# Performance work log

Hardware: AMD Instinct MI355X
Metric: run time of the kernel (lower is better)

Reference implementation:

```python
import jax, jax.numpy as jnp
import numpy as np

DIM = 768
HEADS = 12
DIM_HEAD = 64
INNER = HEADS * DIM_HEAD  # 768
EPS = 1e-5


def setup_inputs() -> dict:
    key = jax.random.key(0)
    ks = jax.random.split(key, 5)
    x = jax.random.normal(ks[0], (4, 2048, DIM), dtype=jnp.float32)
    ln_g = jnp.ones((DIM,), dtype=jnp.float32)
    ln_b = jnp.zeros((DIM,), dtype=jnp.float32)
    s1 = 1.0 / np.sqrt(DIM)
    W_qkv = jax.random.uniform(ks[1], (DIM, 3 * INNER), dtype=jnp.float32, minval=-s1, maxval=s1)
    b_qkv = jax.random.uniform(ks[2], (3 * INNER,), dtype=jnp.float32, minval=-s1, maxval=s1)
    s2 = 1.0 / np.sqrt(INNER)
    W_out = jax.random.uniform(ks[3], (INNER, DIM), dtype=jnp.float32, minval=-s2, maxval=s2)
    b_out = jax.random.uniform(ks[4], (DIM,), dtype=jnp.float32, minval=-s2, maxval=s2)
    return {"x": x, "ln_g": ln_g, "ln_b": ln_b, "W_qkv": W_qkv, "b_qkv": b_qkv, "W_out": W_out, "b_out": b_out}


def reference(x, ln_g, ln_b, W_qkv, b_qkv, W_out, b_out):
    b, n, _ = x.shape
    # pre-norm LayerNorm
    mu = jnp.mean(x, axis=-1, keepdims=True)
    var = jnp.mean(jnp.square(x - mu), axis=-1, keepdims=True)
    xn = (x - mu) * jax.lax.rsqrt(var + EPS) * ln_g + ln_b
    qkv = xn @ W_qkv + b_qkv  # [b, n, 3*inner]
    q, k, v = jnp.split(qkv, 3, axis=-1)
    def to_heads(t):
        return t.reshape(b, n, HEADS, DIM_HEAD).transpose(0, 2, 1, 3)  # b h n d
    q, k, v = map(to_heads, (q, k, v))
    q = q * (DIM_HEAD ** -0.5)
    sim = jnp.einsum('bhid,bhjd->bhij', q, k)
    attn = jax.nn.softmax(sim, axis=-1)  # dropout is identity (p=0.0)
    out = jnp.einsum('bhij,bhjd->bhid', attn, v)
    out = out.transpose(0, 2, 1, 3).reshape(b, n, INNER)
    return out @ W_out + b_out
```

## Files before the change

kernel.cpp:

```cpp
#include <hip/hip_runtime.h>
#include <cstdint>
#include <cstddef>


#define SEQ    2048
#define NBATCH 4
#define DMODEL 768
#define NHEADS 12
#define DHEAD  64
#define MROWS  (NBATCH * SEQ)
#define NQKV   (3 * DMODEL)
#define KT     64
#define NT     (SEQ / KT)

using f32x4  = __attribute__((ext_vector_type(4))) float;
using u16x8  = __attribute__((ext_vector_type(8))) unsigned short;
using s16x8  = __attribute__((ext_vector_type(8))) short;
using u16x4  = __attribute__((ext_vector_type(4))) unsigned short;
using s16x4  = __attribute__((ext_vector_type(4))) short;

__device__ __forceinline__ unsigned short f2bf(float f) {
  union { float f; unsigned int u; } x; x.f = f;
  unsigned int r = x.u + 0x7fffu + ((x.u >> 16) & 1u);
  return (unsigned short)(r >> 16);
}

#if defined(__has_builtin)
#if __has_builtin(__builtin_amdgcn_cvt_pk_bf16_f32)
#define HAVE_PK_BF16 1
#endif
#if __has_builtin(__builtin_amdgcn_exp2f)
#define HAVE_EXP2 1
#endif
#if __has_builtin(__builtin_amdgcn_mfma_f32_16x16x16bf16_1k)
#define HAVE_MFMA_16X16X16_BF16 1
#endif
#endif

__device__ __forceinline__ unsigned int pk_bf16(float a, float b) {
#ifdef HAVE_PK_BF16
  auto v = __builtin_amdgcn_cvt_pk_bf16_f32(a, b);
  union { decltype(v) v2; unsigned int u; } c; c.v2 = v; return c.u;
#else
  return (unsigned int)f2bf(a) | ((unsigned int)f2bf(b) << 16);
#endif
}

__device__ __forceinline__ float fexp2(float x) {
#ifdef HAVE_EXP2
  return __builtin_amdgcn_exp2f(x);
#else
  return exp2f(x);
#endif
}

__device__ __forceinline__ f32x4 mfma16(u16x8 a, u16x8 b, f32x4 c) {
  return __builtin_amdgcn_mfma_f32_16x16x32_bf16((s16x8)a, (s16x8)b, c, 0, 0, 0);
}

__device__ __forceinline__ f32x4 mfma16k16(u16x4 a, u16x4 b, f32x4 c) {
#ifdef HAVE_MFMA_16X16X16_BF16
  return __builtin_amdgcn_mfma_f32_16x16x16bf16_1k((s16x4)a, (s16x4)b, c, 0, 0, 0);
#else
  f32x4 d;
  asm("v_mfma_f32_16x16x16_bf16 %0, %1, %2, %3"
      : "=v"(d) : "v"(a), "v"(b), "v"(c));
  return d;
#endif
}

__device__ __forceinline__ void gl_lds16(const void* g, void* l) {
  __builtin_amdgcn_global_load_lds(
      (const __attribute__((address_space(1))) void*)g,
      (__attribute__((address_space(3))) void*)l, 16, 0, 0);
}

__global__ __launch_bounds__(256) void ln_kernel(
    const float* __restrict__ x, const float* __restrict__ g,
    const float* __restrict__ bb, unsigned short* __restrict__ xn) {
  __shared__ float red[8];
  const int row = blockIdx.x, t = threadIdx.x;
  const float* xr = x + (size_t)row * DMODEL;
  float v0 = xr[t], v1 = xr[t + 256], v2 = xr[t + 512];
  float s = v0 + v1 + v2;
#pragma unroll
  for (int o = 32; o; o >>= 1) s += __shfl_down(s, o);
  if ((t & 63) == 0) red[t >> 6] = s;
  __syncthreads();
  float mu = (red[0] + red[1] + red[2] + red[3]) * (1.0f / DMODEL);
  float d0 = v0 - mu, d1 = v1 - mu, d2 = v2 - mu;
  float q = d0 * d0 + d1 * d1 + d2 * d2;
#pragma unroll
  for (int o = 32; o; o >>= 1) q += __shfl_down(q, o);
  if ((t & 63) == 0) red[4 + (t >> 6)] = q;
  __syncthreads();
  float var = (red[4] + red[5] + red[6] + red[7]) * (1.0f / DMODEL);
  float rstd = rsqrtf(var + 1e-5f);
  size_t base = (size_t)row * DMODEL;
  xn[base + t]       = f2bf(d0 * rstd * g[t]       + bb[t]);
  xn[base + t + 256] = f2bf(d1 * rstd * g[t + 256] + bb[t + 256]);
  xn[base + t + 512] = f2bf(d2 * rstd * g[t + 512] + bb[t + 512]);
}

__global__ __launch_bounds__(256) void tconv_kernel(
    const float* __restrict__ W, unsigned short* __restrict__ Wt, int N) {
  __shared__ float tile[32][33];
  const int n0 = blockIdx.x * 32, k0 = blockIdx.y * 32;
  const int tx = threadIdx.x & 31, ty = threadIdx.x >> 5;
#pragma unroll
  for (int r = 0; r < 4; ++r)
    tile[ty + r * 8][tx] = W[(size_t)(k0 + ty + r * 8) * N + n0 + tx];
  __syncthreads();
#pragma unroll
  for (int r = 0; r < 4; ++r)
    Wt[(size_t)(n0 + ty + r * 8) * DMODEL + k0 + tx] = f2bf(tile[tx][ty + r * 8]);
}

__global__ __launch_bounds__(256, 2) void gemm_qk_kernel(
    const unsigned short* __restrict__ Wt, const unsigned short* __restrict__ xn,
    const float* __restrict__ bias, unsigned short* __restrict__ qb,
    unsigned short* __restrict__ kb) {
  __shared__ alignas(16) unsigned short As[128 * 64];
  __shared__ alignas(16) unsigned short Bs[128 * 64];
  const int t = threadIdx.x, wid = t >> 6, l = t & 63, quad = l >> 4, ll = l & 15;
  const int a0 = blockIdx.x * 128;
  const int b0 = blockIdx.y * 128;
  const int wa = (wid >> 1) * 64, wb = (wid & 1) * 64;
  const int srow = l >> 3, sblk = (l & 7) ^ srow;
  f32x4 acc[4][4] = {};
  for (int k0 = 0; k0 < DMODEL; k0 += 64) {
#pragma unroll
    for (int cc = 0; cc < 4; ++cc) {
      int call = wid * 4 + cc;
      int r = call * 8 + srow;
      gl_lds16(Wt + (size_t)(a0 + r) * DMODEL + k0 + sblk * 8, &As[call * 512]);
      gl_lds16(xn + (size_t)(b0 + r) * DMODEL + k0 + sblk * 8, &Bs[call * 512]);
    }
    __syncthreads();
#pragma unroll
    for (int ks = 0; ks < 2; ++ks) {
      u16x8 af[4], bf[4];
#pragma unroll
      for (int i = 0; i < 4; ++i) {
        int ra = wa + i * 16 + ll, rb = wb + i * 16 + ll;
        int blk = (ks * 4 + quad) ^ (ll & 7);
        af[i] = *(const u16x8*)&As[ra * 64 + blk * 8];
        bf[i] = *(const u16x8*)&Bs[rb * 64 + blk * 8];
      }
#pragma unroll
      for (int mi = 0; mi < 4; ++mi)
#pragma unroll
        for (int ni = 0; ni < 4; ++ni)
          acc[mi][ni] = mfma16(af[mi], bf[ni], acc[mi][ni]);
    }
    __syncthreads();
  }
  const bool isq = (a0 < DMODEL);
  unsigned short* dst = isq ? qb : kb;
  const float sc = isq ? 0.18033688f : 1.0f;
#pragma unroll
  for (int mi = 0; mi < 4; ++mi) {
    int row0 = a0 + wa + mi * 16 + quad * 4;
    float4 bv = *(const float4*)&bias[row0];
    int rr = isq ? row0 : row0 - DMODEL;
    int h = rr >> 6, d0 = rr & 63;
#pragma unroll
    for (int ni = 0; ni < 4; ++ni) {
      int seq = b0 + wb + ni * 16 + ll;
      int b = seq >> 11, i = seq & 2047;
      uint2 pk;
      pk.x = pk_bf16((acc[mi][ni][0] + bv.x) * sc, (acc[mi][ni][1] + bv.y) * sc);
      pk.y = pk_bf16((acc[mi][ni][2] + bv.z) * sc, (acc[mi][ni][3] + bv.w) * sc);
      *(uint2*)&dst[(size_t)((b * NHEADS + h) * SEQ + i) * DHEAD + d0] = pk;
    }
  }
}

__global__ __launch_bounds__(256, 2) void gemm_v_kernel(
    const unsigned short* __restrict__ A, const unsigned short* __restrict__ Bt,
    const float* __restrict__ bias, unsigned short* __restrict__ vt) {
  __shared__ alignas(16) unsigned short As[128 * 64];
  __shared__ alignas(16) unsigned short Bs[128 * 64];
  const int t = threadIdx.x, wid = t >> 6, l = t & 63, quad = l >> 4, ll = l & 15;
  const int m0 = blockIdx.x * 128;
  const int n0 = 2 * DMODEL + blockIdx.y * 128;
  const int wm = (wid >> 1) * 64, wn = (wid & 1) * 64;
  const int srow = l >> 3, sblk = (l & 7) ^ srow;
  f32x4 acc[4][4] = {};
  for (int k0 = 0; k0 < DMODEL; k0 += 64) {
#pragma unroll
    for (int cc = 0; cc < 4; ++cc) {
      int call = wid * 4 + cc;
      int r = call * 8 + srow;
      gl_lds16(A  + (size_t)(m0 + r) * DMODEL + k0 + sblk * 8, &As[call * 512]);
      gl_lds16(Bt + (size_t)(n0 + r) * DMODEL + k0 + sblk * 8, &Bs[call * 512]);
    }
    __syncthreads();
#pragma unroll
    for (int ks = 0; ks < 2; ++ks) {
      u16x8 af[4], bf[4];
#pragma unroll
      for (int i = 0; i < 4; ++i) {
        int ra = wm + i * 16 + ll, rb = wn + i * 16 + ll;
        int blk = (ks * 4 + quad) ^ (ll & 7);
        af[i] = *(const u16x8*)&As[ra * 64 + blk * 8];
        bf[i] = *(const u16x8*)&Bs[rb * 64 + blk * 8];
      }
#pragma unroll
      for (int mi = 0; mi < 4; ++mi)
#pragma unroll
        for (int ni = 0; ni < 4; ++ni)
          acc[mi][ni] = mfma16(af[mi], bf[ni], acc[mi][ni]);
    }
    __syncthreads();
  }
#pragma unroll
  for (int mi = 0; mi < 4; ++mi) {
    int gm = m0 + wm + mi * 16 + quad * 4;
    int b = gm >> 11, i0 = gm & 2047;
#pragma unroll
    for (int ni = 0; ni < 4; ++ni) {
      int gn = n0 + wn + ni * 16 + ll;
      float bv = bias[gn];
      int rem = gn - 2 * DMODEL;
      int h = rem >> 6, d = rem & 63;
      int bh = b * NHEADS + h;
      uint2 pk;
      pk.x = pk_bf16(acc[mi][ni][0] + bv, acc[mi][ni][1] + bv);
      pk.y = pk_bf16(acc[mi][ni][2] + bv, acc[mi][ni][3] + bv);
      *(uint2*)&vt[((size_t)bh * DHEAD + d) * SEQ + i0] = pk;
    }
  }
}

__global__ __launch_bounds__(256, 3) void attn_kernel(
    const unsigned short* __restrict__ qbuf, const unsigned short* __restrict__ kbuf,
    const unsigned short* __restrict__ vtg, unsigned short* __restrict__ ao) {
  __shared__ alignas(16) unsigned short stage[2][2][KT * DHEAD];
  const int t = threadIdx.x, wid = t >> 6, l = t & 63, quad = l >> 4, ll = l & 15;
  const int Lid = blockIdx.y * 16 + blockIdx.x;
  const int w = (Lid & 7) * 96 + (Lid >> 3);
  const int qt = w & 15, bh = w >> 4;
  const unsigned short* qg  = qbuf + ((size_t)bh * SEQ + qt * 128) * DHEAD;
  const unsigned short* kg0 = kbuf + (size_t)bh * SEQ * DHEAD;
  const unsigned short* vt0 = vtg  + (size_t)bh * DHEAD * SEQ;
  const int srow = l >> 3;
  const int sblk = (l & 7) ^ srow;

  unsigned short* Qs = &stage[0][0][0];
#pragma unroll
  for (int cc = 0; cc < 4; ++cc) {
    int call = wid * 4 + cc;
    gl_lds16(qg + (call * 8 + srow) * 64 + sblk * 8, Qs + call * 512);
  }
  __syncthreads();
  u16x8 qf[2][2];
#pragma unroll
  for (int mi = 0; mi < 2; ++mi)
#pragma unroll
    for (int ks = 0; ks < 2; ++ks) {
      int r = wid * 32 + mi * 16 + ll;
      int blk = (ks * 4 + quad) ^ (ll & 7);
      qf[mi][ks] = *(const u16x8*)&Qs[r * 64 + blk * 8];
    }
  __syncthreads();

  auto stage_tile = [&](int buf, int kt2) {
    const unsigned short* kg = kg0 + (size_t)kt2 * KT * DHEAD;
#pragma unroll
    for (int c = 0; c < 2; ++c) {
      int call = wid * 2 + c;
      int r = call * 8 + srow;
      gl_lds16(kg + r * 64 + sblk * 8, &stage[buf][0][call * 512]);
      gl_lds16(vt0 + (size_t)r * SEQ + kt2 * KT + sblk * 8, &stage[buf][1][call * 512]);
    }
  };

  f32x4 oacc[2][4] = {};
  f32x4 osum[2] = {};
  const u16x4 onesb = {0x3f80u, 0x3f80u, 0x3f80u, 0x3f80u};

  stage_tile(0, 0);
  int buf = 0;
  for (int kt2 = 0; kt2 < NT; ++kt2) {
    __syncthreads();
    if (kt2 + 1 < NT) stage_tile(buf ^ 1, kt2 + 1);
    const unsigned short* Ks = &stage[buf][0][0];
    const unsigned short* Vs = &stage[buf][1][0];

    f32x4 st[2][4] = {};
#pragma unroll
    for (int ks = 0; ks < 2; ++ks)
#pragma unroll
      for (int ni = 0; ni < 4; ++ni) {
        int r = ni * 16 + ll;
        int blk = (ks * 4 + quad) ^ (ll & 7);
        u16x8 kf = *(const u16x8*)&Ks[r * 64 + blk * 8];
        st[0][ni] = mfma16(kf, qf[0][ks], st[0][ni]);
        st[1][ni] = mfma16(kf, qf[1][ks], st[1][ni]);
      }

#pragma unroll
    for (int ni = 0; ni < 4; ++ni) {
      u16x4 pf[2];
#pragma unroll
      for (int mi = 0; mi < 2; ++mi) {
        float p0 = fexp2(st[mi][ni][0]);
        float p1 = fexp2(st[mi][ni][1]);
        float p2 = fexp2(st[mi][ni][2]);
        float p3 = fexp2(st[mi][ni][3]);
        union { uint2 u; u16x4 v; } cv;
        cv.u.x = pk_bf16(p0, p1);
        cv.u.y = pk_bf16(p2, p3);
        pf[mi] = cv.v;
        osum[mi] = mfma16k16(pf[mi], onesb, osum[mi]);
      }
      const int voff = (((ni * 2 + (quad >> 1)) ^ (ll & 7)) << 3) + (quad & 1) * 4;
#pragma unroll
      for (int di = 0; di < 4; ++di) {
        u16x4 vf = *(const u16x4*)&Vs[(di * 16 + ll) * 64 + voff];
        oacc[0][di] = mfma16k16(pf[0], vf, oacc[0][di]);
        oacc[1][di] = mfma16k16(pf[1], vf, oacc[1][di]);
      }
    }
    buf ^= 1;
  }

  const int b = bh / NHEADS, h = bh - b * NHEADS;
#pragma unroll
  for (int mi = 0; mi < 2; ++mi) {
#pragma unroll
    for (int r = 0; r < 4; ++r) {
      float inv = 1.0f / osum[mi][r];
      int row = qt * 128 + wid * 32 + mi * 16 + quad * 4 + r;
      size_t base = ((size_t)(b * SEQ + row)) * DMODEL + h * DHEAD;
#pragma unroll
      for (int di = 0; di < 4; ++di)
        ao[base + di * 16 + ll] = f2bf(oacc[mi][di][r] * inv);
    }
  }
}

__global__ __launch_bounds__(256, 2) void gemm_out_kernel(
    const unsigned short* __restrict__ Wt, const unsigned short* __restrict__ ao,
    const float* __restrict__ bias, float* __restrict__ out) {
  __shared__ alignas(16) unsigned short As[128 * 64];
  __shared__ alignas(16) unsigned short Bs[128 * 64];
  const int t = threadIdx.x, wid = t >> 6, l = t & 63, quad = l >> 4, ll = l & 15;
  const int a0 = blockIdx.x * 128;
  const int b0 = blockIdx.y * 128;
  const int wa = (wid >> 1) * 64, wb = (wid & 1) * 64;
  const int srow = l >> 3, sblk = (l & 7) ^ srow;
  f32x4 acc[4][4] = {};
  for (int k0 = 0; k0 < DMODEL; k0 += 64) {
#pragma unroll
    for (int cc = 0; cc < 4; ++cc) {
      int call = wid * 4 + cc;
      int r = call * 8 + srow;
      gl_lds16(Wt + (size_t)(a0 + r) * DMODEL + k0 + sblk * 8, &As[call * 512]);
      gl_lds16(ao + (size_t)(b0 + r) * DMODEL + k0 + sblk * 8, &Bs[call * 512]);
    }
    __syncthreads();
#pragma unroll
    for (int ks = 0; ks < 2; ++ks) {
      u16x8 af[4], bf[4];
#pragma unroll
      for (int i = 0; i < 4; ++i) {
        int ra = wa + i * 16 + ll, rb = wb + i * 16 + ll;
        int blk = (ks * 4 + quad) ^ (ll & 7);
        af[i] = *(const u16x8*)&As[ra * 64 + blk * 8];
        bf[i] = *(const u16x8*)&Bs[rb * 64 + blk * 8];
      }
#pragma unroll
      for (int mi = 0; mi < 4; ++mi)
#pragma unroll
        for (int ni = 0; ni < 4; ++ni)
          acc[mi][ni] = mfma16(af[mi], bf[ni], acc[mi][ni]);
    }
    __syncthreads();
  }
#pragma unroll
  for (int mi = 0; mi < 4; ++mi) {
    int row0 = a0 + wa + mi * 16 + quad * 4;
    float4 bv = *(const float4*)&bias[row0];
#pragma unroll
    for (int ni = 0; ni < 4; ++ni) {
      int seq = b0 + wb + ni * 16 + ll;
      float4 o;
      o.x = acc[mi][ni][0] + bv.x;
      o.y = acc[mi][ni][1] + bv.y;
      o.z = acc[mi][ni][2] + bv.z;
      o.w = acc[mi][ni][3] + bv.w;
      *(float4*)&out[(size_t)seq * DMODEL + row0] = o;
    }
  }
}

extern "C" void kernel_launch(void* const* d_in, const int* in_sizes, int n_in,
                              void* d_out, int out_size, void* d_ws, size_t ws_size,
                              hipStream_t stream) {
  const float* x     = (const float*)d_in[0];
  const float* ln_g  = (const float*)d_in[1];
  const float* ln_b  = (const float*)d_in[2];
  const float* W_qkv = (const float*)d_in[3];
  const float* b_qkv = (const float*)d_in[4];
  const float* W_out = (const float*)d_in[5];
  const float* b_out = (const float*)d_in[6];
  float* out = (float*)d_out;

  char* ws = (char*)d_ws;
  unsigned short* xn    = (unsigned short*)(ws);
  unsigned short* wqkvt = (unsigned short*)(ws + 12582912);
  unsigned short* woutt = (unsigned short*)(ws + 16121856);
  unsigned short* qb    = (unsigned short*)(ws + 17301504);
  unsigned short* kb    = (unsigned short*)(ws + 29884416);
  unsigned short* vt    = (unsigned short*)(ws + 42467328);
  unsigned short* ao    = xn;

  ln_kernel<<<MROWS, 256, 0, stream>>>(x, ln_g, ln_b, xn);
  tconv_kernel<<<dim3(NQKV / 32, DMODEL / 32), 256, 0, stream>>>(W_qkv, wqkvt, NQKV);
  tconv_kernel<<<dim3(DMODEL / 32, DMODEL / 32), 256, 0, stream>>>(W_out, woutt, DMODEL);
  gemm_qk_kernel<<<dim3(12, 64), 256, 0, stream>>>(wqkvt, xn, b_qkv, qb, kb);
  gemm_v_kernel<<<dim3(64, 6), 256, 0, stream>>>(xn, wqkvt, b_qkv, vt);
  attn_kernel<<<dim3(SEQ / 128, NBATCH * NHEADS), 256, 0, stream>>>(qb, kb, vt, ao);
  gemm_out_kernel<<<dim3(6, 64), 256, 0, stream>>>(woutt, ao, b_out, out);
}
```

Before: 247.4 us.

## Merge QK and V GEMMs, widen attention blocks to 8 waves, halve out-GEMM tile

Folds the separate QK and V projection GEMMs into one launch of 1152 blocks with a remapped block index, removing a launch and the tail gap between them. The attention kernel now runs 512 threads per block, with each wave owning 16 query rows instead of 32. This cuts per-wave registers and raises occupancy, at the cost of less K/V reuse per wave. The output GEMM uses 64x128 tiles to double the block count and fill more CUs, which gives lower arithmetic intensity per tile.

```diff
diff --git a/kernel.cpp b/kernel.cpp
--- a/kernel.cpp
+++ b/kernel.cpp
@@ -116,15 +116,21 @@
     Wt[(size_t)(n0 + ty + r * 8) * DMODEL + k0 + tx] = f2bf(tile[tx][ty + r * 8]);
 }
 
-__global__ __launch_bounds__(256, 2) void gemm_qk_kernel(
+__global__ __launch_bounds__(256, 2) void gemm_qkv_kernel(
     const unsigned short* __restrict__ Wt, const unsigned short* __restrict__ xn,
     const float* __restrict__ bias, unsigned short* __restrict__ qb,
-    unsigned short* __restrict__ kb) {
+    unsigned short* __restrict__ kb, unsigned short* __restrict__ vt) {
   __shared__ alignas(16) unsigned short As[128 * 64];
   __shared__ alignas(16) unsigned short Bs[128 * 64];
   const int t = threadIdx.x, wid = t >> 6, l = t & 63, quad = l >> 4, ll = l & 15;
-  const int a0 = blockIdx.x * 128;
-  const int b0 = blockIdx.y * 128;
+  const int bid = blockIdx.x;
+  const int w = (bid & 7) * 144 + (bid >> 3);
+  const bool isqk = (w < 768);
+  int a0, b0;
+  if (isqk) { a0 = (w % 12) * 128; b0 = (w / 12) * 128; }
+  else { int w2 = w - 768; a0 = (w2 & 63) * 128; b0 = 2 * DMODEL + (w2 >> 6) * 128; }
+  const unsigned short* Ap = isqk ? (Wt + (size_t)a0 * DMODEL) : (xn + (size_t)a0 * DMODEL);
+  const unsigned short* Bp = isqk ? (xn + (size_t)b0 * DMODEL) : (Wt + (size_t)b0 * DMODEL);
   const int wa = (wid >> 1) * 64, wb = (wid & 1) * 64;
   const int srow = l >> 3, sblk = (l & 7) ^ srow;
   f32x4 acc[4][4] = {};
@@ -133,8 +139,8 @@
     for (int cc = 0; cc < 4; ++cc) {
       int call = wid * 4 + cc;
       int r = call * 8 + srow;
-      gl_lds16(Wt + (size_t)(a0 + r) * DMODEL + k0 + sblk * 8, &As[call * 512]);
-      gl_lds16(xn + (size_t)(b0 + r) * DMODEL + k0 + sblk * 8, &Bs[call * 512]);
+      gl_lds16(Ap + (size_t)r * DMODEL + k0 + sblk * 8, &As[call * 512]);
+      gl_lds16(Bp + (size_t)r * DMODEL + k0 + sblk * 8, &Bs[call * 512]);
     }
     __syncthreads();
 #pragma unroll
@@ -155,85 +161,48 @@
     }
     __syncthreads();
   }
-  const bool isq = (a0 < DMODEL);
-  unsigned short* dst = isq ? qb : kb;
-  const float sc = isq ? 0.18033688f : 1.0f;
-#pragma unroll
-  for (int mi = 0; mi < 4; ++mi) {
-    int row0 = a0 + wa + mi * 16 + quad * 4;
-    float4 bv = *(const float4*)&bias[row0];
-    int rr = isq ? row0 : row0 - DMODEL;
-    int h = rr >> 6, d0 = rr & 63;
-#pragma unroll
-    for (int ni = 0; ni < 4; ++ni) {
-      int seq = b0 + wb + ni * 16 + ll;
-      int b = seq >> 11, i = seq & 2047;
-      uint2 pk;
-      pk.x = pk_bf16((acc[mi][ni][0] + bv.x) * sc, (acc[mi][ni][1] + bv.y) * sc);
-      pk.y = pk_bf16((acc[mi][ni][2] + bv.z) * sc, (acc[mi][ni][3] + bv.w) * sc);
-      *(uint2*)&dst[(size_t)((b * NHEADS + h) * SEQ + i) * DHEAD + d0] = pk;
-    }
-  }
-}
-
-__global__ __launch_bounds__(256, 2) void gemm_v_kernel(
-    const unsigned short* __restrict__ A, const unsigned short* __restrict__ Bt,
-    const float* __restrict__ bias, unsigned short* __restrict__ vt) {
-  __shared__ alignas(16) unsigned short As[128 * 64];
-  __shared__ alignas(16) unsigned short Bs[128 * 64];
-  const int t = threadIdx.x, wid = t >> 6, l = t & 63, quad = l >> 4, ll = l & 15;
-  const int m0 = blockIdx.x * 128;
-  const int n0 = 2 * DMODEL + blockIdx.y * 128;
-  const int wm = (wid >> 1) * 64, wn = (wid & 1) * 64;
-  const int srow = l >> 3, sblk = (l & 7) ^ srow;
-  f32x4 acc[4][4] = {};
-  for (int k0 = 0; k0 < DMODEL; k0 += 64) {
-#pragma unroll
-    for (int cc = 0; cc < 4; ++cc) {
-      int call = wid * 4 + cc;
-      int r = call * 8 + srow;
-      gl_lds16(A  + (size_t)(m0 + r) * DMODEL + k0 + sblk * 8, &As[call * 512]);
-      gl_lds16(Bt + (size_t)(n0 + r) * DMODEL + k0 + sblk * 8, &Bs[call * 512]);
-    }
-    __syncthreads();
-#pragma unroll
-    for (int ks = 0; ks < 2; ++ks) {
-      u16x8 af[4], bf[4];
-#pragma unroll
-      for (int i = 0; i < 4; ++i) {
-        int ra = wm + i * 16 + ll, rb = wn + i * 16 + ll;
-        int blk = (ks * 4 + quad) ^ (ll & 7);
-        af[i] = *(const u16x8*)&As[ra * 64 + blk * 8];
-        bf[i] = *(const u16x8*)&Bs[rb * 64 + blk * 8];
-      }
-#pragma unroll
-      for (int mi = 0; mi < 4; ++mi)
-#pragma unroll
-        for (int ni = 0; ni < 4; ++ni)
-          acc[mi][ni] = mfma16(af[mi], bf[ni], acc[mi][ni]);
-    }
-    __syncthreads();
-  }
-#pragma unroll
-  for (int mi = 0; mi < 4; ++mi) {
-    int gm = m0 + wm + mi * 16 + quad * 4;
-    int b = gm >> 11, i0 = gm & 2047;
-#pragma unroll
-    for (int ni = 0; ni < 4; ++ni) {
-      int gn = n0 + wn + ni * 16 + ll;
-      float bv = bias[gn];
-      int rem = gn - 2 * DMODEL;
-      int h = rem >> 6, d = rem & 63;
-      int bh = b * NHEADS + h;
-      uint2 pk;
-      pk.x = pk_bf16(acc[mi][ni][0] + bv, acc[mi][ni][1] + bv);
-      pk.y = pk_bf16(acc[mi][ni][2] + bv, acc[mi][ni][3] + bv);
-      *(uint2*)&vt[((size_t)bh * DHEAD + d) * SEQ + i0] = pk;
-    }
-  }
-}
-
-__global__ __launch_bounds__(256, 3) void attn_kernel(
+  if (isqk) {
+    const bool isq = (a0 < DMODEL);
+    unsigned short* dst = isq ? qb : kb;
+    const float sc = isq ? 0.18033688f : 1.0f;
+#pragma unroll
+    for (int mi = 0; mi < 4; ++mi) {
+      int row0 = a0 + wa + mi * 16 + quad * 4;
+      float4 bv = *(const float4*)&bias[row0];
+      int rr = isq ? row0 : row0 - DMODEL;
+      int h = rr >> 6, d0 = rr & 63;
+#pragma unroll
+      for (int ni = 0; ni < 4; ++ni) {
+        int seq = b0 + wb + ni * 16 + ll;
+        int b = seq >> 11, i = seq & 2047;
+        uint2 pk;
+        pk.x = pk_bf16((acc[mi][ni][0] + bv.x) * sc, (acc[mi][ni][1] + bv.y) * sc);
+        pk.y = pk_bf16((acc[mi][ni][2] + bv.z) * sc, (acc[mi][ni][3] + bv.w) * sc);
+        *(uint2*)&dst[(size_t)((b * NHEADS + h) * SEQ + i) * DHEAD + d0] = pk;
+      }
+    }
+  } else {
+#pragma unroll
+    for (int mi = 0; mi < 4; ++mi) {
+      int gm = a0 + wa + mi * 16 + quad * 4;
+      int b = gm >> 11, i0 = gm & 2047;
+#pragma unroll
+      for (int ni = 0; ni < 4; ++ni) {
+        int gn = b0 + wb + ni * 16 + ll;
+        float bv = bias[gn];
+        int rem = gn - 2 * DMODEL;
+        int h = rem >> 6, d = rem & 63;
+        int bh = b * NHEADS + h;
+        uint2 pk;
+        pk.x = pk_bf16(acc[mi][ni][0] + bv, acc[mi][ni][1] + bv);
+        pk.y = pk_bf16(acc[mi][ni][2] + bv, acc[mi][ni][3] + bv);
+        *(uint2*)&vt[((size_t)bh * DHEAD + d) * SEQ + i0] = pk;
+      }
+    }
+  }
+}
+
+__global__ __launch_bounds__(512, 6) void attn_kernel(
     const unsigned short* __restrict__ qbuf, const unsigned short* __restrict__ kbuf,
     const unsigned short* __restrict__ vtg, unsigned short* __restrict__ ao) {
   __shared__ alignas(16) unsigned short stage[2][2][KT * DHEAD];
@@ -249,35 +218,29 @@
 
   unsigned short* Qs = &stage[0][0][0];
 #pragma unroll
-  for (int cc = 0; cc < 4; ++cc) {
-    int call = wid * 4 + cc;
+  for (int cc = 0; cc < 2; ++cc) {
+    int call = wid * 2 + cc;
     gl_lds16(qg + (call * 8 + srow) * 64 + sblk * 8, Qs + call * 512);
   }
   __syncthreads();
-  u16x8 qf[2][2];
-#pragma unroll
-  for (int mi = 0; mi < 2; ++mi)
-#pragma unroll
-    for (int ks = 0; ks < 2; ++ks) {
-      int r = wid * 32 + mi * 16 + ll;
-      int blk = (ks * 4 + quad) ^ (ll & 7);
-      qf[mi][ks] = *(const u16x8*)&Qs[r * 64 + blk * 8];
-    }
+  u16x8 qf[2];
+#pragma unroll
+  for (int ks = 0; ks < 2; ++ks) {
+    int r = wid * 16 + ll;
+    int blk = (ks * 4 + quad) ^ (ll & 7);
+    qf[ks] = *(const u16x8*)&Qs[r * 64 + blk * 8];
+  }
   __syncthreads();
 
   auto stage_tile = [&](int buf, int kt2) {
     const unsigned short* kg = kg0 + (size_t)kt2 * KT * DHEAD;
-#pragma unroll
-    for (int c = 0; c < 2; ++c) {
-      int call = wid * 2 + c;
-      int r = call * 8 + srow;
-      gl_lds16(kg + r * 64 + sblk * 8, &stage[buf][0][call * 512]);
-      gl_lds16(vt0 + (size_t)r * SEQ + kt2 * KT + sblk * 8, &stage[buf][1][call * 512]);
-    }
+    int r = wid * 8 + srow;
+    gl_lds16(kg + r * 64 + sblk * 8, &stage[buf][0][wid * 512]);
+    gl_lds16(vt0 + (size_t)r * SEQ + kt2 * KT + sblk * 8, &stage[buf][1][wid * 512]);
   };
 
-  f32x4 oacc[2][4] = {};
-  f32x4 osum[2] = {};
+  f32x4 oacc[4] = {};
+  f32x4 osum = {};
   const u16x4 onesb = {0x3f80u, 0x3f80u, 0x3f80u, 0x3f80u};
 
   stage_tile(0, 0);
@@ -288,7 +251,7 @@
     const unsigned short* Ks = &stage[buf][0][0];
     const unsigned short* Vs = &stage[buf][1][0];
 
-    f32x4 st[2][4] = {};
+    f32x4 st[4] = {};
 #pragma unroll
     for (int ks = 0; ks < 2; ++ks)
 #pragma unroll
@@ -296,31 +259,25 @@
         int r = ni * 16 + ll;
         int blk = (ks * 4 + quad) ^ (ll & 7);
         u16x8 kf = *(const u16x8*)&Ks[r * 64 + blk * 8];
-        st[0][ni] = mfma16(kf, qf[0][ks], st[0][ni]);
-        st[1][ni] = mfma16(kf, qf[1][ks], st[1][ni]);
+        st[ni] = mfma16(kf, qf[ks], st[ni]);
       }
 
 #pragma unroll
     for (int ni = 0; ni < 4; ++ni) {
-      u16x4 pf[2];
-#pragma unroll
-      for (int mi = 0; mi < 2; ++mi) {
-        float p0 = fexp2(st[mi][ni][0]);
-        float p1 = fexp2(st[mi][ni][1]);
-        float p2 = fexp2(st[mi][ni][2]);
-        float p3 = fexp2(st[mi][ni][3]);
-        union { uint2 u; u16x4 v; } cv;
-        cv.u.x = pk_bf16(p0, p1);
-        cv.u.y = pk_bf16(p2, p3);
-        pf[mi] = cv.v;
-        osum[mi] = mfma16k16(pf[mi], onesb, osum[mi]);
-      }
+      float p0 = fexp2(st[ni][0]);
+      float p1 = fexp2(st[ni][1]);
+      float p2 = fexp2(st[ni][2]);
+      float p3 = fexp2(st[ni][3]);
+      union { uint2 u; u16x4 v; } cv;
+      cv.u.x = pk_bf16(p0, p1);
+      cv.u.y = pk_bf16(p2, p3);
+      u16x4 pf = cv.v;
+      osum = mfma16k16(pf, onesb, osum);
       const int voff = (((ni * 2 + (quad >> 1)) ^ (ll & 7)) << 3) + (quad & 1) * 4;
 #pragma unroll
       for (int di = 0; di < 4; ++di) {
         u16x4 vf = *(const u16x4*)&Vs[(di * 16 + ll) * 64 + voff];
-        oacc[0][di] = mfma16k16(pf[0], vf, oacc[0][di]);
-        oacc[1][di] = mfma16k16(pf[1], vf, oacc[1][di]);
+        oacc[di] = mfma16k16(pf, vf, oacc[di]);
       }
     }
     buf ^= 1;
@@ -328,51 +285,58 @@
 
   const int b = bh / NHEADS, h = bh - b * NHEADS;
 #pragma unroll
-  for (int mi = 0; mi < 2; ++mi) {
-#pragma unroll
-    for (int r = 0; r < 4; ++r) {
-      float inv = 1.0f / osum[mi][r];
-      int row = qt * 128 + wid * 32 + mi * 16 + quad * 4 + r;
-      size_t base = ((size_t)(b * SEQ + row)) * DMODEL + h * DHEAD;
-#pragma unroll
-      for (int di = 0; di < 4; ++di)
-        ao[base + di * 16 + ll] = f2bf(oacc[mi][di][r] * inv);
-    }
-  }
-}
-
-__global__ __launch_bounds__(256, 2) void gemm_out_kernel(
+  for (int r = 0; r < 4; ++r) {
+    float inv = 1.0f / osum[r];
+    int row = qt * 128 + wid * 16 + quad * 4 + r;
+    size_t base = ((size_t)(b * SEQ + row)) * DMODEL + h * DHEAD;
+#pragma unroll
+    for (int di = 0; di < 4; ++di)
+      ao[base + di * 16 + ll] = f2bf(oacc[di][r] * inv);
+  }
+}
+
+__global__ __launch_bounds__(256, 3) void gemm_out_kernel(
     const unsigned short* __restrict__ Wt, const unsigned short* __restrict__ ao,
     const float* __restrict__ bias, float* __restrict__ out) {
-  __shared__ alignas(16) unsigned short As[128 * 64];
+  __shared__ alignas(16) unsigned short As[64 * 64];
   __shared__ alignas(16) unsigned short Bs[128 * 64];
   const int t = threadIdx.x, wid = t >> 6, l = t & 63, quad = l >> 4, ll = l & 15;
-  const int a0 = blockIdx.x * 128;
+  const int a0 = blockIdx.x * 64;
   const int b0 = blockIdx.y * 128;
-  const int wa = (wid >> 1) * 64, wb = (wid & 1) * 64;
+  const int wa = (wid >> 1) * 32, wb = (wid & 1) * 64;
   const int srow = l >> 3, sblk = (l & 7) ^ srow;
-  f32x4 acc[4][4] = {};
+  f32x4 acc[2][4] = {};
   for (int k0 = 0; k0 < DMODEL; k0 += 64) {
 #pragma unroll
-    for (int cc = 0; cc < 4; ++cc) {
-      int call = wid * 4 + cc;
-      int r = call * 8 + srow;
-      gl_lds16(Wt + (size_t)(a0 + r) * DMODEL + k0 + sblk * 8, &As[call * 512]);
-      gl_lds16(ao + (size_t)(b0 + r) * DMODEL + k0 + sblk * 8, &Bs[call * 512]);
+    for (int cc = 0; cc < 6; ++cc) {
+      int call = wid * 6 + cc;
+      if (call < 8) {
+        int r = call * 8 + srow;
+        gl_lds16(Wt + (size_t)(a0 + r) * DMODEL + k0 + sblk * 8, &As[call * 512]);
+      } else {
+        int c2 = call - 8;
+        int r = c2 * 8 + srow;
+        gl_lds16(ao + (size_t)(b0 + r) * DMODEL + k0 + sblk * 8, &Bs[c2 * 512]);
+      }
     }
     __syncthreads();
 #pragma unroll
     for (int ks = 0; ks < 2; ++ks) {
-      u16x8 af[4], bf[4];
-#pragma unroll
-      for (int i = 0; i < 4; ++i) {
-        int ra = wa + i * 16 + ll, rb = wb + i * 16 + ll;
+      u16x8 af[2], bf[4];
+#pragma unroll
+      for (int i = 0; i < 2; ++i) {
+        int ra = wa + i * 16 + ll;
         int blk = (ks * 4 + quad) ^ (ll & 7);
         af[i] = *(const u16x8*)&As[ra * 64 + blk * 8];
+      }
+#pragma unroll
+      for (int i = 0; i < 4; ++i) {
+        int rb = wb + i * 16 + ll;
+        int blk = (ks * 4 + quad) ^ (ll & 7);
         bf[i] = *(const u16x8*)&Bs[rb * 64 + blk * 8];
       }
 #pragma unroll
-      for (int mi = 0; mi < 4; ++mi)
+      for (int mi = 0; mi < 2; ++mi)
 #pragma unroll
         for (int ni = 0; ni < 4; ++ni)
           acc[mi][ni] = mfma16(af[mi], bf[ni], acc[mi][ni]);
@@ -380,7 +344,7 @@
     __syncthreads();
   }
 #pragma unroll
-  for (int mi = 0; mi < 4; ++mi) {
+  for (int mi = 0; mi < 2; ++mi) {
     int row0 = a0 + wa + mi * 16 + quad * 4;
     float4 bv = *(const float4*)&bias[row0];
 #pragma unroll
@@ -420,8 +384,7 @@
   ln_kernel<<<MROWS, 256, 0, stream>>>(x, ln_g, ln_b, xn);
   tconv_kernel<<<dim3(NQKV / 32, DMODEL / 32), 256, 0, stream>>>(W_qkv, wqkvt, NQKV);
   tconv_kernel<<<dim3(DMODEL / 32, DMODEL / 32), 256, 0, stream>>>(W_out, woutt, DMODEL);
-  gemm_qk_kernel<<<dim3(12, 64), 256, 0, stream>>>(wqkvt, xn, b_qkv, qb, kb);
-  gemm_v_kernel<<<dim3(64, 6), 256, 0, stream>>>(xn, wqkvt, b_qkv, vt);
-  attn_kernel<<<dim3(SEQ / 128, NBATCH * NHEADS), 256, 0, stream>>>(qb, kb, vt, ao);
-  gemm_out_kernel<<<dim3(6, 64), 256, 0, stream>>>(woutt, ao, b_out, out);
-}
+  gemm_qkv_kernel<<<1152, 256, 0, stream>>>(wqkvt, xn, b_qkv, qb, kb, vt);
+  attn_kernel<<<dim3(SEQ / 128, NBATCH * NHEADS), 512, 0, stream>>>(qb, kb, vt, ao);
+  gemm_out_kernel<<<dim3(12, 64), 256, 0, stream>>>(woutt, ao, b_out, out);
+}
```

New measurement: 229.2 us. 7.4% less time.
